# Optimization experiments

Hardware: AMD Instinct MI355X
Metric: run time of the kernel (lower is better)

The kernel has to match this reference:

```python
import jax, jax.numpy as jnp
import numpy as np
from functools import partial

IMG = 800
ANCHOR_SIZES = (32.0, 64.0, 128.0, 256.0, 512.0)
RATIOS = (0.5, 1.0, 2.0)
PRE_NMS = 1000
POST_NMS = 1000
NMS_TH = 0.7
MIN_SIZE = 1e-3
POOL = 7
SRATIO = 2  # roi_align sampling_ratio
SCALES = (0.25, 0.125, 0.0625, 0.03125)
BBOX_CLIP = float(np.log(1000.0 / 16.0))


def _cell_anchors(size):
    r = jnp.asarray(RATIOS, jnp.float32)
    hr = jnp.sqrt(r)
    wr = 1.0 / hr
    ws = size * wr
    hs = size * hr
    return jnp.round(jnp.stack([-ws / 2, -hs / 2, ws / 2, hs / 2], axis=1))  # [A,4]


def _grid_anchors(gh, gw, sh, sw, cell):
    sx = jnp.arange(gw, dtype=jnp.float32) * sw
    sy = jnp.arange(gh, dtype=jnp.float32) * sh
    yy, xx = jnp.meshgrid(sy, sx, indexing='ij')
    shifts = jnp.stack([xx, yy, xx, yy], axis=-1).reshape(-1, 4)
    # order: H-major, W, then A anchors per cell (matches torchvision)
    return (shifts[:, None, :] + cell[None, :, :]).reshape(-1, 4)


def _flatten_level(obj, dl):
    # permute_and_flatten: [B,A,H,W] -> [B,H*W*A], [B,4A,H,W] -> [B,H*W*A,4]
    B, A, H, W = obj.shape
    o = obj.transpose(0, 2, 3, 1).reshape(B, -1)
    d = dl.reshape(B, A, 4, H, W).transpose(0, 3, 4, 1, 2).reshape(B, -1, 4)
    return o, d


def _decode(deltas, anchors):
    # BoxCoder.decode with weights (1,1,1,1)
    w = anchors[:, 2] - anchors[:, 0]
    h = anchors[:, 3] - anchors[:, 1]
    cx = anchors[:, 0] + 0.5 * w
    cy = anchors[:, 1] + 0.5 * h
    dx, dy = deltas[..., 0], deltas[..., 1]
    dw = jnp.minimum(deltas[..., 2], BBOX_CLIP)
    dh = jnp.minimum(deltas[..., 3], BBOX_CLIP)
    pcx = dx * w + cx
    pcy = dy * h + cy
    pw = jnp.exp(dw) * w
    ph = jnp.exp(dh) * h
    return jnp.stack([pcx - 0.5 * pw, pcy - 0.5 * ph, pcx + 0.5 * pw, pcy + 0.5 * ph], axis=-1)


def _iou_one(box, boxes):
    a1 = (box[2] - box[0]) * (box[3] - box[1])
    a2 = (boxes[:, 2] - boxes[:, 0]) * (boxes[:, 3] - boxes[:, 1])
    lt = jnp.maximum(box[:2], boxes[:, :2])
    rb = jnp.minimum(box[2:], boxes[:, 2:])
    wh = jnp.clip(rb - lt, 0.0)
    inter = wh[:, 0] * wh[:, 1]
    return inter / (a1 + a2 - inter)


def _nms(boxes, scores, k):
    # greedy NMS, fixed k iterations (jit-friendly)
    def step(s, _):
        i = jnp.argmax(s)
        sup = _iou_one(boxes[i], boxes) > NMS_TH
        s = jnp.where(sup, -jnp.inf, s).at[i].set(-jnp.inf)
        return s, i
    _, idx = jax.lax.scan(step, scores, None, length=k)
    return idx


def _roi_align(feat, rois, scale):
    # feat [C,H,W], rois [R,4] in image coords -> [R,C,POOL,POOL]; aligned=False semantics
    C, H, W = feat.shape
    R = rois.shape[0]
    x1, y1 = rois[:, 0] * scale, rois[:, 1] * scale
    x2, y2 = rois[:, 2] * scale, rois[:, 3] * scale
    rw = jnp.maximum(x2 - x1, 1.0)
    rh = jnp.maximum(y2 - y1, 1.0)
    S = POOL * SRATIO
    t = (jnp.arange(S, dtype=jnp.float32) + 0.5) / S
    y = jnp.broadcast_to((y1[:, None] + rh[:, None] * t)[:, :, None], (R, S, S))
    x = jnp.broadcast_to((x1[:, None] + rw[:, None] * t)[:, None, :], (R, S, S))
    mask = (y >= -1.0) & (y <= H) & (x >= -1.0) & (x <= W)
    yc = jnp.clip(y, 0.0, H - 1.0)
    xc = jnp.clip(x, 0.0, W - 1.0)
    y0 = jnp.floor(yc).astype(jnp.int32)
    x0 = jnp.floor(xc).astype(jnp.int32)
    y1i = jnp.minimum(y0 + 1, H - 1)
    x1i = jnp.minimum(x0 + 1, W - 1)
    ly = yc - y0
    lx = xc - x0
    v00 = feat[:, y0, x0]
    v01 = feat[:, y0, x1i]
    v10 = feat[:, y1i, x0]
    v11 = feat[:, y1i, x1i]  # [C,R,S,S]
    val = ((1 - ly) * (1 - lx) * v00 + (1 - ly) * lx * v01 + ly * (1 - lx) * v10 + ly * lx * v11) * mask
    pooled = val.reshape(C, R, POOL, SRATIO, POOL, SRATIO).mean(axis=(3, 5))
    return pooled.transpose(1, 0, 2, 3)


def _forward(image_tensors, feats, objs, dls):
    B = image_tensors.shape[0]
    grids = [o.shape[-2:] for o in objs]
    anchors = jnp.concatenate([
        _grid_anchors(gh, gw, float(IMG // gh), float(IMG // gw), _cell_anchors(s))
        for (gh, gw), s in zip(grids, ANCHOR_SIZES)], axis=0)
    flat = [_flatten_level(o, d) for o, d in zip(objs, dls)]
    # RPN detaches both objectness and deltas before proposal filtering
    obj = jax.lax.stop_gradient(jnp.concatenate([f[0] for f in flat], axis=1))   # [B,N]
    dl = jax.lax.stop_gradient(jnp.concatenate([f[1] for f in flat], axis=1))    # [B,N,4]
    proposals = _decode(dl, anchors)                                             # [B,N,4]
    npl = [3 * gh * gw for gh, gw in grids]
    offs = np.concatenate([[0], np.cumsum(npl)])
    idx_parts, lvl_parts = [], []
    for l, n in enumerate(npl):
        k = min(PRE_NMS, n)
        _, ix = jax.lax.top_k(obj[:, offs[l]:offs[l + 1]], k)
        idx_parts.append(ix + offs[l])
        lvl_parts.append(jnp.full((k,), l, jnp.float32))
    idx = jnp.concatenate(idx_parts, axis=1)   # [B,K]
    lvl = jnp.concatenate(lvl_parts)           # [K]
    boxes = jnp.take_along_axis(proposals, idx[..., None], axis=1)
    scores = jax.nn.sigmoid(jnp.take_along_axis(obj, idx, axis=1))
    boxes = jnp.clip(boxes, 0.0, float(IMG))   # clip_boxes_to_image (square image)
    ws = boxes[..., 2] - boxes[..., 0]
    hs = boxes[..., 3] - boxes[..., 1]
    valid = (ws >= MIN_SIZE) & (hs >= MIN_SIZE)  # remove_small_boxes via score masking
    scores = jnp.where(valid, scores, -jnp.inf)
    # batched_nms: offset boxes per level so NMS is independent across levels
    off_boxes = boxes + (lvl * (IMG + 1.0))[None, :, None]
    keep = jax.vmap(lambda b, s: _nms(b, s, POST_NMS))(off_boxes, scores)  # [B,POST]
    props = jnp.take_along_axis(boxes, keep[..., None], axis=1)            # [B,POST,4]
    # MultiScaleRoIAlign level mapping (k0=4, canonical 224)
    area = (props[..., 2] - props[..., 0]) * (props[..., 3] - props[..., 1])
    li = jnp.clip(jnp.floor(4.0 + jnp.log2(jnp.sqrt(area) / 224.0 + 1e-6)), 2.0, 5.0).astype(jnp.int32) - 2
    R = props.shape[1]
    C = feats[0].shape[1]
    box_feats = jnp.zeros((B, R, C, POOL, POOL), feats[0].dtype)
    for l, (f, sc) in enumerate(zip(feats, SCALES)):
        pooled = jax.vmap(partial(_roi_align, scale=sc))(f, props)  # [B,R,C,7,7]
        box_feats = box_feats + pooled * (li == l)[..., None, None, None]
    return props, box_feats.reshape(B * R, C, POOL, POOL)


def setup_inputs() -> dict:
    key = jax.random.key(0)
    ks = jax.random.split(key, 16)
    B, C = 2, 256
    grids = [(200, 200), (100, 100), (50, 50), (25, 25), (13, 13)]
    d = {}
    d['image_tensors'] = jax.random.normal(ks[0], (B, 3, IMG, IMG), jnp.float32)
    for i in range(4):
        gh, gw = grids[i]
        d[f'features_{i}'] = jax.random.normal(ks[1 + i], (B, C, gh, gw), jnp.float32)
    for i in range(5):
        gh, gw = grids[i]
        d[f'objectness_{i}'] = jax.random.normal(ks[5 + i], (B, 3, gh, gw), jnp.float32)
        d[f'pred_bbox_deltas_{i}'] = jax.random.normal(ks[10 + i], (B, 12, gh, gw), jnp.float32)
    return d


def reference(image_tensors, features_0, features_1, features_2, features_3,
              objectness_0, objectness_1, objectness_2, objectness_3, objectness_4,
              pred_bbox_deltas_0, pred_bbox_deltas_1, pred_bbox_deltas_2,
              pred_bbox_deltas_3, pred_bbox_deltas_4):
    feats = [features_0, features_1, features_2, features_3]
    objs = [objectness_0, objectness_1, objectness_2, objectness_3, objectness_4]
    dls = [pred_bbox_deltas_0, pred_bbox_deltas_1, pred_bbox_deltas_2,
           pred_bbox_deltas_3, pred_bbox_deltas_4]
    return _forward(image_tensors, feats, objs, dls)
```

## Files before the change

### kernel.cpp

```cpp
#include <hip/hip_runtime.h>
#include <math.h>

typedef unsigned int u32;
typedef unsigned long long u64;

#define N_ALL 159882
#define NC 4507
#define MROW 72
#define NEGINF_KEY 0x007FFFFFu
#define IMGF 800.0f
#define BBOX_CLIP_F 4.135166556742356f

#define NHWC_L1 10240000u
#define NHWC_L2 12800000u
#define NHWC_L3 13440000u
#define NHWC_BS 13600000u

__constant__ int   c_offs[5]  = {0,120000,150000,157500,159375};
__constant__ int   c_gw[5]    = {200,100,50,25,13};
__constant__ float c_stride[5]= {4.f,8.f,16.f,32.f,61.f};
__constant__ float c_size[5]  = {32.f,64.f,128.f,256.f,512.f};
__constant__ int   c_koff[5]  = {0,1000,2000,3000,4000};
__constant__ int   c_k[5]     = {1000,1000,1000,1000,507};
__constant__ float c_ratio[3] = {0.5f,1.f,2.f};

struct PtrArgs { const float* obj[5]; const float* dl[5]; };

__device__ __forceinline__ u32 fkey32f(float x){
  u32 u = __float_as_uint(x);
  return (u & 0x80000000u) ? ~u : (u | 0x80000000u);
}
__device__ __forceinline__ int level_of(int g){
  return (g >= 159375) ? 4 : (g >= 157500) ? 3 : (g >= 150000) ? 2 : (g >= 120000) ? 1 : 0;
}
__device__ __forceinline__ u64 readlane64(u64 v, int l){
  u32 lo = (u32)v, hi = (u32)(v >> 32);
  u32 a = (u32)__builtin_amdgcn_readlane((int)lo, l);
  u32 b = (u32)__builtin_amdgcn_readlane((int)hi, l);
  return ((u64)b << 32) | (u64)a;
}

__global__ void k_decode(PtrArgs pa, int B, float* boxes_all, u32* key_all, u32* fkey_all){
#pragma clang fp contract(off)
  int idx = blockIdx.x*blockDim.x + threadIdx.x;
  int total = B*N_ALL;
  if (idx >= total) return;
  int b = idx / N_ALL;
  int g = idx - b*N_ALL;
  int l = level_of(g);
  int n = g - c_offs[l];
  int a = n % 3;
  int pos = n / 3;
  int gw = c_gw[l];
  int wx = pos % gw;
  int hy = pos / gw;
  int plane = gw*gw;
  const float* obj = pa.obj[l];
  const float* dl  = pa.dl[l];
  float logit = obj[(size_t)(b*3 + a)*plane + hy*gw + wx];
  size_t dbase = (size_t)(b*12 + a*4)*plane + (size_t)hy*gw + wx;
  float d0 = dl[dbase];
  float d1 = dl[dbase + (size_t)plane];
  float d2 = dl[dbase + (size_t)2*plane];
  float d3 = dl[dbase + (size_t)3*plane];
  float ratio = c_ratio[a];
  float hr = sqrtf(ratio);
  float wr = 1.0f/hr;
  float wsz = c_size[l]*wr;
  float hsz = c_size[l]*hr;
  float ca0 = rintf(-0.5f*wsz), ca1 = rintf(-0.5f*hsz);
  float ca2 = rintf( 0.5f*wsz), ca3 = rintf( 0.5f*hsz);
  float st = c_stride[l];
  float shx = (float)wx*st, shy = (float)hy*st;
  float ax1 = shx+ca0, ay1 = shy+ca1, ax2 = shx+ca2, ay2 = shy+ca3;
  float w = ax2-ax1, h = ay2-ay1;
  float cx = ax1 + 0.5f*w, cy = ay1 + 0.5f*h;
  float dw = fminf(d2, BBOX_CLIP_F), dh = fminf(d3, BBOX_CLIP_F);
  float pcx = d0*w + cx, pcy = d1*h + cy;
  float pw = expf(dw)*w, ph = expf(dh)*h;
  float x1 = pcx - 0.5f*pw, y1 = pcy - 0.5f*ph;
  float x2 = pcx + 0.5f*pw, y2 = pcy + 0.5f*ph;
  x1 = fminf(fmaxf(x1,0.f),IMGF); y1 = fminf(fmaxf(y1,0.f),IMGF);
  x2 = fminf(fmaxf(x2,0.f),IMGF); y2 = fminf(fmaxf(y2,0.f),IMGF);
  bool valid = ((x2-x1) >= 0.001f) && ((y2-y1) >= 0.001f);
  ((float4*)boxes_all)[idx] = make_float4(x1,y1,x2,y2);
  key_all[idx] = fkey32f(logit);
  float sgf = 1.0f/(1.0f + expf(-logit));
  fkey_all[idx] = valid ? fkey32f(sgf) : NEGINF_KEY;
}

__global__ __launch_bounds__(1024) void k_topk(const u32* key_all, u32* cand_g, int B){
  int blk = blockIdx.x;
  int b = blk / 5, l = blk - b*5;
  int g0 = c_offs[l];
  int N  = ((l==4)?N_ALL:c_offs[l+1]) - g0;
  int k  = c_k[l];
  const u32* keys = key_all + (size_t)b*N_ALL + g0;
  u32* out = cand_g + (size_t)b*NC + c_koff[l];
  __shared__ u32 hist[4096];
  __shared__ u64 buf[4096];
  __shared__ int s_bstar, s_chi, s_scnt, s_bcnt;
  int tid = threadIdx.x;
  for (int i=tid;i<4096;i+=1024) hist[i]=0;
  if (tid==0){ s_scnt=0; s_bcnt=0; }
  __syncthreads();
  for (int i=tid;i<N;i+=1024) atomicAdd(&hist[keys[i]>>20], 1u);
  __syncthreads();
  for (int s=1;s<4096;s<<=1){
    u32 v[4];
    for (int j=0;j<4;j++){ int i=tid+j*1024; v[j]=hist[i] + ((i+s<4096)?hist[i+s]:0); }
    __syncthreads();
    for (int j=0;j<4;j++){ int i=tid+j*1024; hist[i]=v[j]; }
    __syncthreads();
  }
  for (int j=0;j<4;j++){
    int i = tid + j*1024;
    u32 suf = hist[i];
    u32 nxt = (i+1<4096)?hist[i+1]:0u;
    if (suf >= (u32)k && nxt < (u32)k){ s_bstar = i; s_chi = (int)nxt; }
  }
  __syncthreads();
  int bstar = s_bstar, chi = s_chi;
  int r = k - chi;
  for (int i=tid;i<N;i+=1024){
    u32 kk = keys[i];
    int bin = (int)(kk>>20);
    if (bin > bstar){
      int slot = atomicAdd(&s_scnt,1);
      out[slot] = (u32)(g0 + i);
    } else if (bin == bstar){
      int slot = atomicAdd(&s_bcnt,1);
      if (slot < 4096) buf[slot] = ((u64)kk<<32) | (u32)(~(u32)(g0+i));
    }
  }
  __syncthreads();
  int m = s_bcnt; if (m > 4096) m = 4096;
  int P = 1; while (P < m) P <<= 1; if (P < 2) P = 2;
  for (int i=m+tid;i<P;i+=1024) buf[i]=0;
  __syncthreads();
  for (u32 ksz=2;ksz<=(u32)P;ksz<<=1){
    for (u32 j=ksz>>1;j>0;j>>=1){
      for (int i=tid;i<P;i+=1024){
        u32 ixj = (u32)i ^ j;
        if (ixj > (u32)i){
          u64 x = buf[i], y = buf[ixj];
          bool up = ((i & ksz) == 0);
          if (up ? (x < y) : (x > y)){ buf[i]=y; buf[ixj]=x; }
        }
      }
      __syncthreads();
    }
  }
  for (int t=tid; t<r && t<m; t+=1024) out[chi + t] = ~(u32)buf[t];
}

__global__ __launch_bounds__(1024) void k_rank(u32* cand_g, const u32* key_all, int B){
  int blk = blockIdx.x; int b = blk/5, l = blk - b*5;
  int k = c_k[l];
  u32* seg = cand_g + (size_t)b*NC + c_koff[l];
  __shared__ u64 sk[1024];
  int tid = threadIdx.x;
  u64 v = 0;
  if (tid < k){
    u32 g = seg[tid];
    v = ((u64)key_all[(size_t)b*N_ALL + g]<<32) | (u32)(~g);
  }
  sk[tid] = v;
  __syncthreads();
  for (u32 ksz=2;ksz<=1024;ksz<<=1){
    for (u32 j=ksz>>1;j>0;j>>=1){
      int i = tid;
      u32 ixj = (u32)i ^ j;
      if (ixj > (u32)i){
        u64 x = sk[i], y = sk[ixj];
        bool up = ((i & ksz) == 0);
        if (up ? (x < y) : (x > y)){ sk[i]=y; sk[ixj]=x; }
      }
      __syncthreads();
    }
  }
  if (tid < k) seg[tid] = ~(u32)sk[tid];
}

__device__ __forceinline__ void merge_elem(const u64* As, const u64* Bs, u64* dst,
                                           int m, int n, int k){
  int lo = k - n; if (lo < 0) lo = 0;
  int hi = (k < m) ? k : m;
  while (lo < hi){
    int mid = (lo + hi) >> 1;
    if (As[mid] > Bs[k-1-mid]) lo = mid + 1; else hi = mid;
  }
  int a = lo, bb = k - lo;
  u64 out;
  if (a < m && (bb >= n || As[a] > Bs[bb])) out = As[a]; else out = Bs[bb];
  dst[k] = out;
}

__global__ __launch_bounds__(1024) void k_sortcand(const u32* cand_g, const u32* fkey_all,
                                                   const float* boxes_all,
                                                   float* sorted_box, float* sorted_off,
                                                   u32* fcnt_ws, float* pos0box){
  __shared__ u64 sA[NC];
  __shared__ u64 sB[NC];
  __shared__ u32 wsum[16];
  __shared__ int s_f;
  int b = blockIdx.x, tid = threadIdx.x;
  int lane = tid & 63, wv = tid >> 6;
  if (tid == 0) s_f = 0;
  size_t cbase = (size_t)b*NC;
  size_t abase = (size_t)b*N_ALL;
  u64 below = lane ? (~0ull >> (64 - lane)) : 0ull;
  for (int l = 0; l < 5; ++l){
    int kl = c_k[l], ko = c_koff[l];
    bool act = tid < kl;
    u32 fk = 0; bool val = false;
    u32 i_g = (u32)(ko + tid);
    if (act){
      u32 g = cand_g[cbase + i_g];
      fk = fkey_all[abase + g];
      val = fk > NEGINF_KEY;
    }
    u64 bal = __ballot(act && val);
    int pv_w = __popcll(bal & below);
    if (lane == 0) wsum[wv] = (u32)__popcll(bal);
    __syncthreads();
    int pre = 0, Vl = 0;
    #pragma unroll
    for (int w2 = 0; w2 < 16; ++w2){
      int s = (int)wsum[w2];
      if (w2 < wv) pre += s;
      Vl += s;
    }
    if (tid == 0) s_f += Vl;
    if (act){
      int pv = pre + pv_w;
      int pos = val ? pv : (Vl + (tid - pv));
      sA[ko + pos] = ((u64)fk << 32) | (u32)(~i_g);
    }
    __syncthreads();
  }
  for (int k = tid; k < NC; k += 1024){
    if (k < 2000)       merge_elem(sA,        sA + 1000, sB,        1000, 1000, k);
    else if (k < 4000)  merge_elem(sA + 2000, sA + 3000, sB + 2000, 1000, 1000, k - 2000);
    else                sB[k] = sA[k];
  }
  __syncthreads();
  for (int k = tid; k < NC; k += 1024){
    if (k < 4000) merge_elem(sB, sB + 2000, sA, 2000, 2000, k);
    else          sA[k] = sB[k];
  }
  __syncthreads();
  for (int k = tid; k < NC; k += 1024){
    merge_elem(sA, sA + 4000, sB, 4000, 507, k);
  }
  __syncthreads();
  for (int i = tid; i < NC; i += 1024){
    u32 posc = ~(u32)sB[i];
    u32 g = cand_g[cbase + posc];
    int lvl = level_of((int)g);
    float4 bx = ((const float4*)boxes_all)[abase + g];
    ((float4*)sorted_box)[cbase + i] = bx;
    float off = 801.0f*(float)lvl;
    ((float4*)sorted_off)[cbase + i] = make_float4(bx.x+off, bx.y+off, bx.z+off, bx.w+off);
  }
  if (tid == 0){
    fcnt_ws[b] = (u32)s_f;
    u32 g0b = cand_g[cbase + 0];
    float4 bx = ((const float4*)boxes_all)[abase + g0b];
    ((float4*)pos0box)[b] = bx;
  }
}

__global__ void k_iou(const float* sorted_off, u64* M){
#pragma clang fp contract(off)
  int i = blockIdx.x, b = blockIdx.y, lane = threadIdx.x;
  const float4* boxes = ((const float4*)sorted_off) + (size_t)b*NC;
  float4 bi = boxes[i];
  float a1 = (bi.z-bi.x)*(bi.w-bi.y);
  u64* row = M + ((size_t)b*NC + i)*MROW;
  for (int w=0; w<71; w++){
    int j = w*64 + lane;
    bool sup = false;
    if (j < NC){
      float4 bj = boxes[j];
      float a2 = (bj.z-bj.x)*(bj.w-bj.y);
      float ltx = fmaxf(bi.x,bj.x), lty = fmaxf(bi.y,bj.y);
      float rbx = fminf(bi.z,bj.z), rby = fminf(bi.w,bj.w);
      float wx = fmaxf(rbx-ltx,0.f), wy = fmaxf(rby-lty,0.f);
      float inter = wx*wy;
      float iou = inter/(a1+a2-inter);
      sup = iou > 0.7f;
    }
    u64 word = __ballot(sup);
    if (lane==0) row[w] = word;
  }
}

#define GETQ2(q) { if (t2){ int jj=__builtin_ctzll(t2); t2&=t2-1; q = &buf[cb][jj*72]; } else q = zbuf; }
__global__ __launch_bounds__(256) void k_nms_tr(const float* sorted_box, const u64* M,
                      const u32* fcnt_ws, const float* pos0box, float* props, int B,
                      const float* f0, const float* f1, const float* f2, const float* f3,
                      float* nhwc, int doTr){
  __shared__ u64 buf[2][64*72];
  __shared__ u64 zbuf[72];
  __shared__ int ki[1000];
  __shared__ int s_kc, s_done;
  int bid = blockIdx.x;
  int tid = threadIdx.x;
  if (bid >= B){
    float (*t)[65] = reinterpret_cast<float(*)[65]>(&buf[0][0]);
    int id = bid - B;
    int b = id / 3328;
    int rem = id - b*3328;
    int P, W; const float* f; u32 loff;
    if (rem < 2500){ W=200; f=f0; loff=0u; }
    else if (rem < 3128){ W=100; f=f1; loff=NHWC_L1; rem -= 2500; }
    else if (rem < 3288){ W=50;  f=f2; loff=NHWC_L2; rem -= 3128; }
    else { W=25; f=f3; loff=NHWC_L3; rem -= 3288; }
    P = W*W;
    int ctile = rem & 3, ptile = rem >> 2;
    int c0 = ctile*64, p0 = ptile*64;
    const float* src = f + (size_t)b*256*P;
    float* dst = nhwc + (size_t)b*NHWC_BS + loff;
    int q   = tid & 15;
    int cl0 = tid >> 4;
    bool vec4ok = ((P & 3) == 0);
    int p = p0 + 4*q;
    float4 v[4];
    #pragma unroll
    for (int k = 0; k < 4; ++k){
      int cl = cl0 + 16*k;
      const float* s = src + (size_t)(c0+cl)*P + p;
      if (vec4ok && (p + 3 < P)){
        v[k] = *(const float4*)s;
      } else {
        v[k].x = (p   < P) ? s[0] : 0.f;
        v[k].y = (p+1 < P) ? s[1] : 0.f;
        v[k].z = (p+2 < P) ? s[2] : 0.f;
        v[k].w = (p+3 < P) ? s[3] : 0.f;
      }
    }
    #pragma unroll
    for (int k = 0; k < 4; ++k){
      int cl = cl0 + 16*k;
      t[cl][4*q+0] = v[k].x; t[cl][4*q+1] = v[k].y;
      t[cl][4*q+2] = v[k].z; t[cl][4*q+3] = v[k].w;
    }
    __syncthreads();
    #pragma unroll
    for (int k = 0; k < 4; ++k){
      int pl = cl0 + 16*k;
      int pp = p0 + pl;
      if (pp < P){
        float4 o = make_float4(t[4*q+0][pl], t[4*q+1][pl],
                               t[4*q+2][pl], t[4*q+3][pl]);
        *(float4*)(dst + (size_t)pp*256 + c0 + 4*q) = o;
      }
    }
    return;
  }
  int b = bid;
  int F = (int)fcnt_ws[b];
  const u64* Mb = M + (size_t)b*NC*MROW;
  int nch = (F + 63) >> 6;
  int lane = tid & 63, wv = tid >> 6;
  if (tid == 0){ s_kc = 0; s_done = (nch == 0) ? 1 : 0; }
  if (tid < 72) zbuf[tid] = 0ull;
  if (nch > 0){
    for (int e = tid; e < 64*72; e += 256){
      int rr = e / 72, wo = e - rr*72;
      int r2 = rr; if (r2 > NC-1) r2 = NC-1;
      buf[0][e] = Mb[(size_t)r2*MROW + wo];
    }
  }
  u64 rg[24];
  if (wv > 0 && nch > 1){
    #pragma unroll
    for (int k = 0; k < 24; ++k){
      int e = (tid - 64) + k*192;
      int rr = e/72, wo = e - rr*72;
      int r2 = 64 + rr; if (r2 > NC-1) r2 = NC-1;
      rg[k] = Mb[(size_t)r2*MROW + wo];
    }
  }
  __syncthreads();
  u64 sup0 = 0, sup1 = 0;
  int kc = 0;
  for (int c = 0; c < nch; ++c){
    int cb = c & 1;
    if (wv > 0){
      if (c + 1 < nch){
        #pragma unroll
        for (int k = 0; k < 24; ++k){
          int e = (tid - 64) + k*192;
          buf[cb^1][e] = rg[k];
        }
      }
      if (c + 2 < nch){
        int base2 = (c + 2) << 6;
        #pragma unroll
        for (int k = 0; k < 24; ++k){
          int e = (tid - 64) + k*192;
          int rr = e/72, wo = e - rr*72;
          int r2 = base2 + rr; if (r2 > NC-1) r2 = NC-1;
          rg[k] = Mb[(size_t)r2*MROW + wo];
        }
      }
    } else if (kc < 1000){
      int base = c << 6;
      int cnt = F - base; if (cnt > 64) cnt = 64;
      u64 supw = (c < 64) ? readlane64(sup0, c) : readlane64(sup1, c - 64);
      u64 alive = ~supw;
      if (cnt < 64) alive &= ((1ull << cnt) - 1ull);
      u64 wrow = buf[cb][lane*72 + c];
      u64 below = lane ? (~0ull >> (64 - lane)) : 0ull;
      u64 colb = wrow & below;
      bool myal = ((alive >> lane) & 1ull) != 0ull;
      u64 kept = __ballot(myal);
      #pragma unroll 1
      for (int it = 0; it < 64; ++it){
        bool kj = myal && ((kept & colb) == 0ull);
        u64 nk = __ballot(kj);
        if (nk == kept) break;
        kept = nk;
      }
      int cnt_k = __popcll(kept);
      int rank  = __popcll(kept & below);
      int budget = 1000 - kc;
      bool sel = ((kept >> lane) & 1ull) && (rank < budget);
      if (sel) ki[kc + rank] = base + lane;
      if (cnt_k >= budget){
        if (lane == 0){ s_done = 1; s_kc = 1000; }
      } else {
        kc += cnt_k;
        u64 t2 = kept;
        while (t2){
          const u64 *q0,*q1,*q2,*q3,*q4,*q5,*q6,*q7;
          const u64 *q8,*q9,*q10,*q11,*q12,*q13,*q14,*q15;
          GETQ2(q0) GETQ2(q1) GETQ2(q2) GETQ2(q3)
          GETQ2(q4) GETQ2(q5) GETQ2(q6) GETQ2(q7)
          GETQ2(q8) GETQ2(q9) GETQ2(q10) GETQ2(q11)
          GETQ2(q12) GETQ2(q13) GETQ2(q14) GETQ2(q15)
          u64 a0=q0[lane],a1=q1[lane],a2=q2[lane],a3=q3[lane];
          u64 a4=q4[lane],a5=q5[lane],a6=q6[lane],a7=q7[lane];
          u64 a8=q8[lane],a9=q9[lane],a10=q10[lane],a11=q11[lane];
          u64 a12=q12[lane],a13=q13[lane],a14=q14[lane],a15=q15[lane];
          sup0 |= (((a0|a1)|(a2|a3))|((a4|a5)|(a6|a7)))
                | (((a8|a9)|(a10|a11))|((a12|a13)|(a14|a15)));
          if (lane < 7){
            u64 b0=q0[64+lane],b1=q1[64+lane],b2=q2[64+lane],b3=q3[64+lane];
            u64 b4=q4[64+lane],b5=q5[64+lane],b6=q6[64+lane],b7=q7[64+lane];
            u64 b8=q8[64+lane],b9=q9[64+lane],b10=q10[64+lane],b11=q11[64+lane];
            u64 b12=q12[64+lane],b13=q13[64+lane],b14=q14[64+lane],b15=q15[64+lane];
            sup1 |= (((b0|b1)|(b2|b3))|((b4|b5)|(b6|b7)))
                  | (((b8|b9)|(b10|b11))|((b12|b13)|(b14|b15)));
          }
        }
        if (lane == 0) s_kc = kc;
      }
    }
    __syncthreads();
    if (s_done) break;
  }
  __syncthreads();
  int kcf = s_kc;
  const float* sb = sorted_box + (size_t)b*NC*4;
  float* pb = props + (size_t)b*4000;
  float4 p0v = ((const float4*)pos0box)[b];
  float pv[4] = {p0v.x, p0v.y, p0v.z, p0v.w};
  for (int idx = tid; idx < 4000; idx += 256){
    int k4 = idx >> 2, comp = idx & 3;
    float v = (k4 < kcf) ? sb[(size_t)ki[k4]*4 + comp] : pv[comp];
    pb[idx] = v;
  }
}

__global__ __launch_bounds__(256, 4) void k_roi_nhwc(const float* nhwc, const float* props,
                                                     float* out){
#pragma clang fp contract(off)
  int r = blockIdx.x;
  int b = r / 1000;
  int tid = threadIdx.x;
  int q = tid & 31;
  int s = tid >> 5;
  __shared__ int   s_o0[196], s_o1[196], s_o2[196], s_o3[196];
  __shared__ float s_a0[196], s_a1[196], s_a2[196], s_a3[196], s_m[196];
  __shared__ float obuf[49*132];
  float bx0 = props[(size_t)r*4+0], by0 = props[(size_t)r*4+1];
  float bx1 = props[(size_t)r*4+2], by1 = props[(size_t)r*4+3];
  float area = (bx1-bx0)*(by1-by0);
  float v = 4.0f + log2f(sqrtf(area)/224.0f + 1e-6f);
  float fl = floorf(v);
  fl = fminf(fmaxf(fl, 2.0f), 5.0f);
  int li = (int)fl - 2;
  int H = (li==0)?200:(li==1)?100:(li==2)?50:25;
  u32 loff = (li==0)?0u:(li==1)?NHWC_L1:(li==2)?NHWC_L2:NHWC_L3;
  float scale = (li==0)?0.25f:(li==1)?0.125f:(li==2)?0.0625f:0.03125f;
  float x1 = bx0*scale, y1 = by0*scale, x2 = bx1*scale, y2 = by1*scale;
  float rw = fmaxf(x2-x1, 1.0f), rh = fmaxf(y2-y1, 1.0f);
  if (tid < 196){
    int syi = tid / 14, sxi = tid - syi*14;
    float ty = ((float)syi + 0.5f)/14.0f;
    float yv = y1 + rh*ty;
    float fy = (yv >= -1.0f && yv <= (float)H) ? 1.0f : 0.0f;
    float yc = fminf(fmaxf(yv,0.0f),(float)(H-1));
    int iy0 = (int)floorf(yc);
    int iy1 = min(iy0+1,H-1);
    float ly = yc-(float)iy0;
    float tx = ((float)sxi + 0.5f)/14.0f;
    float xv = x1 + rw*tx;
    float fx = (xv >= -1.0f && xv <= (float)H) ? 1.0f : 0.0f;
    float xc = fminf(fmaxf(xv,0.0f),(float)(H-1));
    int ix0 = (int)floorf(xc);
    int ix1 = min(ix0+1,H-1);
    float lx = xc-(float)ix0;
    s_o0[tid] = (iy0*H + ix0)*64;
    s_o1[tid] = (iy0*H + ix1)*64;
    s_o2[tid] = (iy1*H + ix0)*64;
    s_o3[tid] = (iy1*H + ix1)*64;
    s_a0[tid] = (1.f-ly)*(1.f-lx);
    s_a1[tid] = (1.f-ly)*lx;
    s_a2[tid] = ly*(1.f-lx);
    s_a3[tid] = ly*lx;
    s_m[tid]  = fy*fx;
  }
  __syncthreads();
  const float4* src4 = (const float4*)(nhwc + (size_t)b*NHWC_BS + loff);
  float4* obuf4 = (float4*)obuf;
  float* orow = out + (size_t)r*12544;
  #pragma unroll 1
  for (int h = 0; h < 2; ++h){
    int qh = h*32 + q;
    for (int p = s; p < 49; p += 8){
      int py = p/7, px = p - py*7;
      float accx = 0.f, accy = 0.f, accz = 0.f, accw = 0.f;
      #pragma unroll
      for (int iy = 0; iy < 2; ++iy){
        #pragma unroll
        for (int ix = 0; ix < 2; ++ix){
          int sp = (py*2+iy)*14 + (px*2+ix);
          int o00 = s_o0[sp], o01 = s_o1[sp], o10 = s_o2[sp], o11 = s_o3[sp];
          float a00 = s_a0[sp], a01 = s_a1[sp], a10 = s_a2[sp], a11 = s_a3[sp];
          float m = s_m[sp];
          float4 v00 = src4[o00 + qh];
          float4 v01 = src4[o01 + qh];
          float4 v10 = src4[o10 + qh];
          float4 v11 = src4[o11 + qh];
          accx += (a00*v00.x + a01*v01.x + a10*v10.x + a11*v11.x)*m;
          accy += (a00*v00.y + a01*v01.y + a10*v10.y + a11*v11.y)*m;
          accz += (a00*v00.z + a01*v01.z + a10*v10.z + a11*v11.z)*m;
          accw += (a00*v00.w + a01*v01.w + a10*v10.w + a11*v11.w)*m;
        }
      }
      obuf4[p*33 + q] = make_float4(accx*0.25f, accy*0.25f, accz*0.25f, accw*0.25f);
    }
    __syncthreads();
    for (int o = tid; o < 6272; o += 256){
      int c = o/49, p = o - c*49;
      orow[h*6272 + o] = obuf[p*132 + c];
    }
    __syncthreads();
  }
}

__global__ __launch_bounds__(256) void k_roi(const float* f0, const float* f1,
                                             const float* f2, const float* f3,
                                             const float* props, float* out){
#pragma clang fp contract(off)
  int r = blockIdx.x;
  int b = r / 1000;
  int tid = threadIdx.x;
  __shared__ float s_ly[14], s_lx[14], s_ym[14], s_xm[14];
  __shared__ int   s_y0[14], s_y1[14], s_x0[14], s_x1[14];
  float bx0 = props[(size_t)r*4+0], by0 = props[(size_t)r*4+1];
  float bx1 = props[(size_t)r*4+2], by1 = props[(size_t)r*4+3];
  float area = (bx1-bx0)*(by1-by0);
  float v = 4.0f + log2f(sqrtf(area)/224.0f + 1e-6f);
  float fl = floorf(v);
  fl = fminf(fmaxf(fl, 2.0f), 5.0f);
  int li = (int)fl - 2;
  const float* fptr = (li==0)?f0:(li==1)?f1:(li==2)?f2:f3;
  int H = (li==0)?200:(li==1)?100:(li==2)?50:25;
  float scale = (li==0)?0.25f:(li==1)?0.125f:(li==2)?0.0625f:0.03125f;
  float x1 = bx0*scale, y1 = by0*scale, x2 = bx1*scale, y2 = by1*scale;
  float rw = fmaxf(x2-x1, 1.0f), rh = fmaxf(y2-y1, 1.0f);
  if (tid < 14){
    float t = ((float)tid + 0.5f)/14.0f;
    float yv = y1 + rh*t;
    s_ym[tid] = (yv >= -1.0f && yv <= (float)H) ? 1.0f : 0.0f;
    float yc = fminf(fmaxf(yv,0.0f),(float)(H-1));
    int iy0 = (int)floorf(yc);
    s_y0[tid]=iy0; s_y1[tid]=min(iy0+1,H-1); s_ly[tid]=yc-(float)iy0;
    float xv = x1 + rw*t;
    s_xm[tid] = (xv >= -1.0f && xv <= (float)H) ? 1.0f : 0.0f;
    float xc = fminf(fmaxf(xv,0.0f),(float)(H-1));
    int ix0 = (int)floorf(xc);
    s_x0[tid]=ix0; s_x1[tid]=min(ix0+1,H-1); s_lx[tid]=xc-(float)ix0;
  }
  __syncthreads();
  size_t plane = (size_t)H*H;
  const float* fb = fptr + (size_t)b*256*plane;
  float* orow = out + (size_t)r*12544;
  for (int o=tid; o<12544; o+=256){
    int c = o/49;
    int p = o - c*49;
    int py = p/7, px = p - py*7;
    const float* fc = fb + (size_t)c*plane;
    float sum = 0.f;
    for (int iy=0; iy<2; iy++){
      int syi = py*2+iy;
      int yy0 = s_y0[syi], yy1 = s_y1[syi];
      float ly = s_ly[syi], fy = s_ym[syi];
      for (int ix=0; ix<2; ix++){
        int sxi = px*2+ix;
        int xx0 = s_x0[sxi], xx1 = s_x1[sxi];
        float lx = s_lx[sxi], fx = s_xm[sxi];
        float v00 = fc[yy0*H+xx0], v01 = fc[yy0*H+xx1];
        float v10 = fc[yy1*H+xx0], v11 = fc[yy1*H+xx1];
        float val = ((1.f-ly)*(1.f-lx)*v00 + (1.f-ly)*lx*v01
                   + ly*(1.f-lx)*v10 + ly*lx*v11) * (fy*fx);
        sum += val;
      }
    }
    orow[o] = sum*0.25f;
  }
}

extern "C" void kernel_launch(void* const* d_in, const int* in_sizes, int n_in,
                              void* d_out, int out_size, void* d_ws, size_t ws_size,
                              hipStream_t stream) {
  int B = in_sizes[0] / (3*800*800);
  PtrArgs pa;
  bool interleaved = (n_in >= 7) && (in_sizes[6] == 4*in_sizes[5]);
  for (int i=0;i<5;i++){
    if (interleaved){
      pa.obj[i] = (const float*)d_in[5+2*i];
      pa.dl[i]  = (const float*)d_in[6+2*i];
    } else {
      pa.obj[i] = (const float*)d_in[5+i];
      pa.dl[i]  = (const float*)d_in[10+i];
    }
  }

  auto align256 = [](size_t x){ return (x + 255) & ~(size_t)255; };
  size_t sz_M      = align256(((size_t)B*NC + 1)*MROW*8);
  size_t sz_boxes  = align256((size_t)B*N_ALL*16);
  size_t sz_key    = align256((size_t)B*N_ALL*4);
  size_t sz_fkey   = align256((size_t)B*N_ALL*4);
  size_t sz_cand   = align256((size_t)B*NC*4);
  size_t sz_sbox   = align256((size_t)B*NC*16);
  size_t sz_soff   = align256((size_t)B*NC*16);
  size_t sz_fcnt   = align256((size_t)B*4);
  size_t sz_p0     = align256((size_t)B*16);
  size_t need = sz_M+sz_boxes+sz_key+sz_fkey+sz_cand+sz_sbox+sz_soff+sz_fcnt+sz_p0;
  size_t outBytes = (size_t)out_size * 4;
  size_t start = (outBytes - need) & ~(size_t)255;
  char* w = (char*)d_out + start;
  auto alloc = [&](size_t bytes)->char*{ char* p = w; w += bytes; return p; };

  u64*  M          = (u64*) alloc(sz_M);
  float* boxes_all = (float*)alloc(sz_boxes);
  u32*  key_all    = (u32*) alloc(sz_key);
  u32*  fkey_all   = (u32*) alloc(sz_fkey);
  u32*  cand_g     = (u32*) alloc(sz_cand);
  float* sorted_box= (float*)alloc(sz_sbox);
  float* sorted_off= (float*)alloc(sz_soff);
  u32*  fcnt       = (u32*) alloc(sz_fcnt);
  float* pos0box   = (float*)alloc(sz_p0);

  float* props     = (float*)d_out;
  float* feats_out = (float*)d_out + (size_t)B*1000*4;

  int total = B*N_ALL;
  k_decode<<<(total+255)/256, 256, 0, stream>>>(pa, B, boxes_all, key_all, fkey_all);
  k_topk<<<B*5, 1024, 0, stream>>>(key_all, cand_g, B);
  k_rank<<<B*5, 1024, 0, stream>>>(cand_g, key_all, B);
  k_sortcand<<<B, 1024, 0, stream>>>(cand_g, fkey_all, boxes_all, sorted_box, sorted_off, fcnt, pos0box);
  k_iou<<<dim3(NC, B), 64, 0, stream>>>(sorted_off, M);

  size_t nhwcBytes = (size_t)B * NHWC_BS * 4;
  int doTr = (ws_size >= nhwcBytes) ? 1 : 0;
  float* nhwc = (float*)d_ws;
  int grid = B + (doTr ? B*3328 : 0);
  k_nms_tr<<<grid, 256, 0, stream>>>(sorted_box, M, fcnt, pos0box, props, B,
                                     (const float*)d_in[1], (const float*)d_in[2],
                                     (const float*)d_in[3], (const float*)d_in[4],
                                     nhwc, doTr);
  if (doTr){
    k_roi_nhwc<<<B*1000, 256, 0, stream>>>(nhwc, props, feats_out);
  } else {
    k_roi<<<B*1000, 256, 0, stream>>>((const float*)d_in[1], (const float*)d_in[2],
                                      (const float*)d_in[3], (const float*)d_in[4],
                                      props, feats_out);
  }
}
```

Baseline: 312.6 us.

## Split per-level top-k into global histogram, select, parallel emit and finalize kernels

Replaces the single-block-per-level top-k kernel with a pipeline. The decode kernel now builds a global 16-bit key histogram with atomics, a select kernel finds the threshold bin, an emit kernel spread over 16 blocks per level compacts the winners and ties using wave ballots, and a finalize kernel bitonic-sorts the tie bin. This is meant to remove the serial scan of up to 120k keys done by only 10 blocks, but it adds a zeroing kernel, extra launches, global atomics in decode, and a larger scratch region.

```diff
diff --git a/kernel.cpp b/kernel.cpp
--- a/kernel.cpp
+++ b/kernel.cpp
@@ -10,6 +10,7 @@
 #define NEGINF_KEY 0x007FFFFFu
 #define IMGF 800.0f
 #define BBOX_CLIP_F 4.135166556742356f
+#define EMIT_S 16
 
 #define NHWC_L1 10240000u
 #define NHWC_L2 12800000u
@@ -40,7 +41,15 @@
   return ((u64)b << 32) | (u64)a;
 }
 
-__global__ void k_decode(PtrArgs pa, int B, float* boxes_all, u32* key_all, u32* fkey_all){
+__global__ void k_zero(u32* ghist, u32* wcnt, u32* tcnt, int B){
+  int n = B*5*65536;
+  int idx = blockIdx.x*blockDim.x + threadIdx.x;
+  for (int i = idx; i < n; i += gridDim.x*blockDim.x) ghist[i] = 0;
+  if (idx < B*5){ wcnt[idx] = 0; tcnt[idx] = 0; }
+}
+
+__global__ void k_decode(PtrArgs pa, int B, float* boxes_all, u32* key_all, u32* fkey_all,
+                         u32* ghist){
 #pragma clang fp contract(off)
   int idx = blockIdx.x*blockDim.x + threadIdx.x;
   int total = B*N_ALL;
@@ -84,74 +93,124 @@
   x2 = fminf(fmaxf(x2,0.f),IMGF); y2 = fminf(fmaxf(y2,0.f),IMGF);
   bool valid = ((x2-x1) >= 0.001f) && ((y2-y1) >= 0.001f);
   ((float4*)boxes_all)[idx] = make_float4(x1,y1,x2,y2);
-  key_all[idx] = fkey32f(logit);
+  u32 key = fkey32f(logit);
+  key_all[idx] = key;
+  atomicAdd(&ghist[(size_t)(b*5 + l)*65536 + (key >> 16)], 1u);
   float sgf = 1.0f/(1.0f + expf(-logit));
   fkey_all[idx] = valid ? fkey32f(sgf) : NEGINF_KEY;
 }
 
-__global__ __launch_bounds__(1024) void k_topk(const u32* key_all, u32* cand_g, int B){
-  int blk = blockIdx.x;
-  int b = blk / 5, l = blk - b*5;
+__global__ __launch_bounds__(1024) void k_sel(const u32* ghist, int2* meta, int B){
+  int bl = blockIdx.x;
+  int l = bl % 5;
+  int k = c_k[l];
+  const u32* h = ghist + (size_t)bl*65536;
+  __shared__ u32 ssum[1024];
+  __shared__ int2 s_meta;
+  int tid = threadIdx.x;
+  u32 cnt[64];
+  u32 tot = 0;
+  const uint4* h4 = (const uint4*)(h + tid*64);
+  #pragma unroll
+  for (int j = 0; j < 16; ++j){
+    uint4 v = h4[j];
+    cnt[4*j+0]=v.x; cnt[4*j+1]=v.y; cnt[4*j+2]=v.z; cnt[4*j+3]=v.w;
+    tot += v.x+v.y+v.z+v.w;
+  }
+  ssum[tid] = tot;
+  __syncthreads();
+  for (int s = 1; s < 1024; s <<= 1){
+    u32 v = ssum[tid] + ((tid+s < 1024) ? ssum[tid+s] : 0);
+    __syncthreads(); ssum[tid] = v; __syncthreads();
+  }
+  u32 run = (tid+1 < 1024) ? ssum[tid+1] : 0;
+  #pragma unroll
+  for (int j = 63; j >= 0; --j){
+    u32 cur = run + cnt[j];
+    if (cur >= (u32)k && run < (u32)k){ s_meta.x = tid*64 + j; s_meta.y = (int)run; }
+    run = cur;
+  }
+  __syncthreads();
+  if (tid == 0) meta[bl] = s_meta;
+}
+
+__global__ __launch_bounds__(1024) void k_emit(const u32* key_all, const int2* meta,
+                                               u32* cand_g, u32* wcnt, u32* tcnt,
+                                               u64* tbuf, int B){
+  int bid = blockIdx.x;
+  int bl = bid / EMIT_S, c = bid - bl*EMIT_S;
+  int b = bl / 5, l = bl - b*5;
   int g0 = c_offs[l];
   int N  = ((l==4)?N_ALL:c_offs[l+1]) - g0;
-  int k  = c_k[l];
+  int CH = (N + EMIT_S - 1)/EMIT_S;
+  int st = c*CH, en = st + CH; if (en > N) en = N;
+  if (st >= en) return;
+  u32 bstar = (u32)meta[bl].x;
   const u32* keys = key_all + (size_t)b*N_ALL + g0;
   u32* out = cand_g + (size_t)b*NC + c_koff[l];
-  __shared__ u32 hist[4096];
+  u64* tb = tbuf + (size_t)bl*4096;
+  int tid = threadIdx.x;
+  int lane = tid & 63;
+  u64 below = lane ? (~0ull >> (64 - lane)) : 0ull;
+  for (int i0 = st; i0 < en; i0 += 1024){
+    int i = i0 + tid;
+    bool inb = (i < en);
+    u32 kk = inb ? keys[i] : 0u;
+    u32 bin = kk >> 16;
+    bool isW = inb && (bin > bstar);
+    bool isT = inb && (bin == bstar);
+    u64 wb = __ballot(isW);
+    if (wb){
+      int wn = __popcll(wb);
+      int b0 = 0;
+      if (lane == 0) b0 = (int)atomicAdd(&wcnt[bl], (u32)wn);
+      b0 = __shfl(b0, 0);
+      if (isW) out[b0 + __popcll(wb & below)] = (u32)(g0 + i);
+    }
+    u64 tbm = __ballot(isT);
+    if (tbm){
+      int tn = __popcll(tbm);
+      int b0 = 0;
+      if (lane == 0) b0 = (int)atomicAdd(&tcnt[bl], (u32)tn);
+      b0 = __shfl(b0, 0);
+      if (isT){
+        int slot = b0 + __popcll(tbm & below);
+        if (slot < 4096) tb[slot] = ((u64)kk << 32) | (u32)(~(u32)(g0 + i));
+      }
+    }
+  }
+}
+
+__global__ __launch_bounds__(1024) void k_fin(const int2* meta, const u32* tcnt,
+                                              const u64* tbuf, u32* cand_g, int B){
+  int bl = blockIdx.x;
+  int b = bl/5, l = bl - b*5;
+  int k = c_k[l];
+  int chi = meta[bl].y;
+  int r = k - chi;
+  u32* out = cand_g + (size_t)b*NC + c_koff[l];
   __shared__ u64 buf[4096];
-  __shared__ int s_bstar, s_chi, s_scnt, s_bcnt;
   int tid = threadIdx.x;
-  for (int i=tid;i<4096;i+=1024) hist[i]=0;
-  if (tid==0){ s_scnt=0; s_bcnt=0; }
-  __syncthreads();
-  for (int i=tid;i<N;i+=1024) atomicAdd(&hist[keys[i]>>20], 1u);
-  __syncthreads();
-  for (int s=1;s<4096;s<<=1){
-    u32 v[4];
-    for (int j=0;j<4;j++){ int i=tid+j*1024; v[j]=hist[i] + ((i+s<4096)?hist[i+s]:0); }
-    __syncthreads();
-    for (int j=0;j<4;j++){ int i=tid+j*1024; hist[i]=v[j]; }
-    __syncthreads();
-  }
-  for (int j=0;j<4;j++){
-    int i = tid + j*1024;
-    u32 suf = hist[i];
-    u32 nxt = (i+1<4096)?hist[i+1]:0u;
-    if (suf >= (u32)k && nxt < (u32)k){ s_bstar = i; s_chi = (int)nxt; }
-  }
-  __syncthreads();
-  int bstar = s_bstar, chi = s_chi;
-  int r = k - chi;
-  for (int i=tid;i<N;i+=1024){
-    u32 kk = keys[i];
-    int bin = (int)(kk>>20);
-    if (bin > bstar){
-      int slot = atomicAdd(&s_scnt,1);
-      out[slot] = (u32)(g0 + i);
-    } else if (bin == bstar){
-      int slot = atomicAdd(&s_bcnt,1);
-      if (slot < 4096) buf[slot] = ((u64)kk<<32) | (u32)(~(u32)(g0+i));
-    }
-  }
-  __syncthreads();
-  int m = s_bcnt; if (m > 4096) m = 4096;
+  int m = (int)tcnt[bl]; if (m > 4096) m = 4096;
   int P = 1; while (P < m) P <<= 1; if (P < 2) P = 2;
-  for (int i=m+tid;i<P;i+=1024) buf[i]=0;
-  __syncthreads();
-  for (u32 ksz=2;ksz<=(u32)P;ksz<<=1){
-    for (u32 j=ksz>>1;j>0;j>>=1){
-      for (int i=tid;i<P;i+=1024){
+  const u64* tb = tbuf + (size_t)bl*4096;
+  for (int i = tid; i < m; i += 1024) buf[i] = tb[i];
+  for (int i = m + tid; i < P; i += 1024) buf[i] = 0;
+  __syncthreads();
+  for (u32 ksz = 2; ksz <= (u32)P; ksz <<= 1){
+    for (u32 j = ksz >> 1; j > 0; j >>= 1){
+      for (int i = tid; i < P; i += 1024){
         u32 ixj = (u32)i ^ j;
         if (ixj > (u32)i){
           u64 x = buf[i], y = buf[ixj];
           bool up = ((i & ksz) == 0);
-          if (up ? (x < y) : (x > y)){ buf[i]=y; buf[ixj]=x; }
+          if (up ? (x < y) : (x > y)){ buf[i] = y; buf[ixj] = x; }
         }
       }
       __syncthreads();
     }
   }
-  for (int t=tid; t<r && t<m; t+=1024) out[chi + t] = ~(u32)buf[t];
+  for (int t = tid; t < r && t < m; t += 1024) out[chi + t] = ~(u32)buf[t];
 }
 
 __global__ __launch_bounds__(1024) void k_rank(u32* cand_g, const u32* key_all, int B){
@@ -652,7 +711,13 @@
   size_t sz_soff   = align256((size_t)B*NC*16);
   size_t sz_fcnt   = align256((size_t)B*4);
   size_t sz_p0     = align256((size_t)B*16);
-  size_t need = sz_M+sz_boxes+sz_key+sz_fkey+sz_cand+sz_sbox+sz_soff+sz_fcnt+sz_p0;
+  size_t sz_ghist  = align256((size_t)B*5*65536*4);
+  size_t sz_meta   = align256((size_t)B*5*8);
+  size_t sz_wcnt   = align256((size_t)B*5*4);
+  size_t sz_tcnt   = align256((size_t)B*5*4);
+  size_t sz_tbuf   = align256((size_t)B*5*4096*8);
+  size_t need = sz_M+sz_boxes+sz_key+sz_fkey+sz_cand+sz_sbox+sz_soff+sz_fcnt+sz_p0
+              + sz_ghist+sz_meta+sz_wcnt+sz_tcnt+sz_tbuf;
   size_t outBytes = (size_t)out_size * 4;
   size_t start = (outBytes - need) & ~(size_t)255;
   char* w = (char*)d_out + start;
@@ -667,13 +732,21 @@
   float* sorted_off= (float*)alloc(sz_soff);
   u32*  fcnt       = (u32*) alloc(sz_fcnt);
   float* pos0box   = (float*)alloc(sz_p0);
+  u32*  ghist      = (u32*) alloc(sz_ghist);
+  int2* meta       = (int2*)alloc(sz_meta);
+  u32*  wcnt       = (u32*) alloc(sz_wcnt);
+  u32*  tcnt       = (u32*) alloc(sz_tcnt);
+  u64*  tbuf       = (u64*) alloc(sz_tbuf);
 
   float* props     = (float*)d_out;
   float* feats_out = (float*)d_out + (size_t)B*1000*4;
 
   int total = B*N_ALL;
-  k_decode<<<(total+255)/256, 256, 0, stream>>>(pa, B, boxes_all, key_all, fkey_all);
-  k_topk<<<B*5, 1024, 0, stream>>>(key_all, cand_g, B);
+  k_zero<<<2560, 256, 0, stream>>>(ghist, wcnt, tcnt, B);
+  k_decode<<<(total+255)/256, 256, 0, stream>>>(pa, B, boxes_all, key_all, fkey_all, ghist);
+  k_sel<<<B*5, 1024, 0, stream>>>(ghist, meta, B);
+  k_emit<<<B*5*EMIT_S, 1024, 0, stream>>>(key_all, meta, cand_g, wcnt, tcnt, tbuf, B);
+  k_fin<<<B*5, 1024, 0, stream>>>(meta, tcnt, tbuf, cand_g, B);
   k_rank<<<B*5, 1024, 0, stream>>>(cand_g, key_all, B);
   k_sortcand<<<B, 1024, 0, stream>>>(cand_g, fkey_all, boxes_all, sorted_box, sorted_off, fcnt, pos0box);
   k_iou<<<dim3(NC, B), 64, 0, stream>>>(sorted_off, M);
```

Measured after the change: 366.3 us. +17.2%, slower.
